# Performance work log

Measured on AMD Instinct MI355X. Metric: run time of the kernel, lower is better.

Reference implementation:

```python
import jax, jax.numpy as jnp
import numpy as np

NUM_NODES = 100000
NUM_REL = 237
D = 200            # entity_out_dim_1 * nheads_GAT_1 = 100*2
C = 50             # conv_out_channels
B = 8192           # batch of (h, r, t) triples


def setup_inputs() -> dict:
    key = jax.random.key(0)
    ks = jax.random.split(key, 8)
    heads = jax.random.randint(ks[0], (B, 1), 0, NUM_NODES)
    rels = jax.random.randint(ks[1], (B, 1), 0, NUM_REL)
    tails = jax.random.randint(ks[2], (B, 1), 0, NUM_NODES)
    batch_inputs = jnp.concatenate([heads, rels, tails], axis=1).astype(jnp.int64)
    return {
        "batch_inputs": batch_inputs,
        "final_entity_embeddings": jax.random.normal(ks[3], (NUM_NODES, D), jnp.float32),
        "final_relation_embeddings": jax.random.normal(ks[4], (NUM_REL, D), jnp.float32),
        "W_ent2rel": jax.random.normal(ks[5], (NUM_REL, D, D), jnp.float32) * (1.0 / np.sqrt(D)),
        "conv_w": jax.random.normal(ks[6], (C, 3), jnp.float32) * 0.5,
        "conv_b": jnp.zeros((C,), jnp.float32),
        "fc_w": jax.random.normal(ks[7], (1, C * D), jnp.float32) * (1.0 / np.sqrt(C * D)),
        "fc_b": jnp.zeros((1,), jnp.float32),
    }


def reference(batch_inputs, final_entity_embeddings, final_relation_embeddings,
              W_ent2rel, conv_w, conv_b, fc_w, fc_b):
    h_idx, r_idx, t_idx = batch_inputs[:, 0], batch_inputs[:, 1], batch_inputs[:, 2]
    src = final_entity_embeddings[h_idx]        # [B, D]
    rel = final_relation_embeddings[r_idx]      # [B, D]
    tail = final_entity_embeddings[t_idx]       # [B, D]
    W = W_ent2rel[r_idx]                        # [B, D, D] per-edge relation transform
    # bmm([B,1,D], [B,D,D]) -> [B,1,D], nonlinearity_ent2rel = tanh
    src = jnp.tanh(jnp.einsum('bd,bde->be', src, W))
    tail = jnp.tanh(jnp.einsum('bd,bde->be', tail, W))
    # ConvKB: stack triple as length-3 sequence, Conv2d kernel (1,3) over seq
    stacked = jnp.stack([src, rel, tail], axis=1)            # [B, 3, D]
    conv = jnp.einsum('bkd,ck->bcd', stacked, conv_w) + conv_b[None, :, None]
    conv = jax.nn.relu(conv)                                  # dropout p=0.0 (eval)
    flat = conv.reshape(conv.shape[0], -1)                    # [B, C*D] (C-major, matches torch view)
    out = flat @ fc_w.T + fc_b                                # [B, 1]
    return out
```

## Files before the change

kernel.cpp:

```cpp
#include <hip/hip_runtime.h>
#include <hip/hip_bf16.h>
#include <math.h>

#define DDIM 200
#define D4   50
#define CCH  50
#define NREL 237
#define MAXE 8
#define MAXR 16
#define NT   256
#define KT   7
#define NTI  13
#define KTKG 28
#define NCOLP 208
#define OSTRIDE 204
#define PACK_UNITS (NREL * KTKG * NCOLP)

typedef __attribute__((ext_vector_type(8))) short bf16x8;
typedef __attribute__((ext_vector_type(4))) float f32x4;

__device__ __forceinline__ uint f2bf(float x) {
    __hip_bfloat16 h = __float2bfloat16(x);
    return (uint)*reinterpret_cast<ushort*>(&h);
}

__global__ __launch_bounds__(256) void packW_kernel(
    const float* __restrict__ W, ushort* __restrict__ Wpk)
{
    const int u = blockIdx.x * 256 + threadIdx.x;
    if (u >= PACK_UNITS) return;
    const int col  = u % NCOLP;
    const int rk   = u / NCOLP;
    const int ktkg = rk % KTKG;
    const int r    = rk / KTKG;
    const int k0   = ktkg * 8;
    uint4 pk = {0u, 0u, 0u, 0u};
    if (col < DDIM) {
        const float* base = W + (size_t)r * DDIM * DDIM + col;
        uint vv[8];
        #pragma unroll
        for (int j = 0; j < 8; ++j) {
            const int k = k0 + j;
            vv[j] = (k < DDIM) ? f2bf(base[(size_t)k * DDIM]) : 0u;
        }
        pk.x = vv[0] | (vv[1] << 16);
        pk.y = vv[2] | (vv[3] << 16);
        pk.z = vv[4] | (vv[5] << 16);
        pk.w = vv[6] | (vv[7] << 16);
    }
    *(uint4*)&Wpk[(size_t)u * 8] = pk;
}

__global__ __launch_bounds__(1024) void relsort_kernel(
    const int* __restrict__ bi, int B, int nblk,
    int* __restrict__ perm, int* __restrict__ blk_r,
    int* __restrict__ blk_start, int* __restrict__ blk_cnt)
{
    __shared__ int hist[NREL];
    __shared__ int offs[NREL];
    __shared__ int wsum[16], wsum2[16];
    const int tid  = threadIdx.x;
    const int lane = tid & 63;
    const int w    = tid >> 6;

    if (tid < NREL) hist[tid] = 0;
    __syncthreads();
    for (int i = tid; i < B; i += 1024)
        atomicAdd(&hist[bi[i * 3 + 1]], 1);
    __syncthreads();

    const int v  = (tid < NREL) ? hist[tid] : 0;
    const int v2 = (tid < NREL) ? (v + MAXE - 1) / MAXE : 0;
    int s = v, s2 = v2;
    #pragma unroll
    for (int off = 1; off < 64; off <<= 1) {
        const int u  = __shfl_up(s,  off, 64);
        const int u2 = __shfl_up(s2, off, 64);
        if (lane >= off) { s += u; s2 += u2; }
    }
    if (lane == 63) { wsum[w] = s; wsum2[w] = s2; }
    __syncthreads();
    int base = 0, base2 = 0;
    for (int i = 0; i < w; ++i) { base += wsum[i]; base2 += wsum2[i]; }
    const int my_off  = base  + s  - v;
    const int my_boff = base2 + s2 - v2;
    if (tid < NREL) offs[tid] = my_off;
    __syncthreads();

    for (int i = tid; i < nblk; i += 1024) blk_cnt[i] = 0;
    if (tid < NREL && v > 0) {
        const int nb = (v + MAXE - 1) / MAXE;
        const int cb = v / nb, ext = v - cb * nb;
        int pos = my_off;
        for (int j = 0; j < nb; ++j) {
            const int c = cb + (j < ext ? 1 : 0);
            blk_r[my_boff + j]     = tid;
            blk_start[my_boff + j] = pos;
            blk_cnt[my_boff + j]   = c;
            pos += c;
        }
    }
    __syncthreads();
    for (int i = tid; i < B; i += 1024) {
        const int pos = atomicAdd(&offs[bi[i * 3 + 1]], 1);
        perm[pos] = i;
    }
}

template <bool PACKED>
__global__ __launch_bounds__(NT) void spkbgat_mfma_kernel(
    const int*   __restrict__ bi,
    const float* __restrict__ ent,
    const float* __restrict__ rel_emb,
    const float* __restrict__ W,
    const ushort* __restrict__ Wpk,
    const float* __restrict__ conv_w,
    const float* __restrict__ conv_b,
    const float* __restrict__ fc_w,
    const float* __restrict__ fc_b,
    const int*   __restrict__ perm,
    const int*   __restrict__ blk_r,
    const int*   __restrict__ blk_start,
    const int*   __restrict__ blk_cnt,
    int nblk,
    float*       __restrict__ out)
{
    __shared__ __align__(16) ushort Ash[KTKG * MAXR * 8];
    __shared__ __align__(16) float  Osh[MAXR][OSTRIDE];
    __shared__ __align__(16) float4 rl4[D4];
    __shared__ __align__(16) float  cwb[CCH][4];
    __shared__ int eid_lds[MAXR];
    __shared__ int bix_lds[MAXE];

    const int tid  = threadIdx.x;
    const int w    = tid >> 6;
    const int lane = tid & 63;
    const int l16  = lane & 15;
    const int kg   = lane >> 4;

    const int bid = blockIdx.x;
    const int q = nblk >> 3, rmd = nblk & 7;
    const int xcd = bid & 7, idx = bid >> 3;
    const int gidx = (xcd < rmd ? xcd * (q + 1) : rmd * (q + 1) + (xcd - rmd) * q) + idx;

    const int cnt = blk_cnt[gidx];
    if (cnt == 0) return;

    const int r     = blk_r[gidx];
    const int start = blk_start[gidx];
    const int rows  = 2 * cnt;

    if (tid < CCH) {
        cwb[tid][0] = conv_w[tid * 3 + 0];
        cwb[tid][1] = conv_w[tid * 3 + 1];
        cwb[tid][2] = conv_w[tid * 3 + 2];
        cwb[tid][3] = conv_b[tid];
    }
    if (tid < D4) rl4[tid] = ((const float4*)rel_emb)[r * D4 + tid];
    if (tid < MAXE) {
        const int b = (tid < cnt) ? perm[start + tid] : -1;
        bix_lds[tid] = b;
        const int bb = (b >= 0) ? b : 0;
        eid_lds[2 * tid]     = bi[3 * bb + 0];
        eid_lds[2 * tid + 1] = bi[3 * bb + 2];
    }
    __syncthreads();

    for (int u = tid; u < KTKG * MAXR; u += NT) {
        const int row  = u & (MAXR - 1);
        const int ktkg = u >> 4;
        uint4 pk = {0u, 0u, 0u, 0u};
        if (ktkg < 25 && row < rows) {
            const float* xp = ent + (size_t)eid_lds[row] * DDIM + ktkg * 8;
            const float4 x0 = *(const float4*)xp;
            const float4 x1 = *(const float4*)(xp + 4);
            pk.x = f2bf(x0.x) | (f2bf(x0.y) << 16);
            pk.y = f2bf(x0.z) | (f2bf(x0.w) << 16);
            pk.z = f2bf(x1.x) | (f2bf(x1.y) << 16);
            pk.w = f2bf(x1.z) | (f2bf(x1.w) << 16);
        }
        *(uint4*)&Ash[u * 8] = pk;
    }
    __syncthreads();

    const int nslots = (w == 0) ? 4 : 3;
    const float*  __restrict__ Wr = W + (size_t)r * DDIM * DDIM;
    const ushort* __restrict__ Wp = Wpk + (size_t)r * KTKG * NCOLP * 8;
    f32x4 acc[4];
    #pragma unroll
    for (int s = 0; s < 4; ++s) acc[s] = (f32x4){0.f, 0.f, 0.f, 0.f};

    for (int kt = 0; kt < KT; ++kt) {
        const int ktkg = kt * 4 + kg;
        const bf16x8 a0 = *(const bf16x8*)&Ash[(ktkg * MAXR + l16) * 8];
        #pragma unroll
        for (int s = 0; s < 4; ++s) {
            if (s < nslots) {
                const int col = (w + 4 * s) * 16 + l16;
                bf16x8 bf;
                if (PACKED) {
                    bf = *(const bf16x8*)&Wp[((size_t)ktkg * NCOLP + col) * 8];
                } else {
                    const int k0 = ktkg * 8;
                    #pragma unroll
                    for (int j = 0; j < 8; ++j) {
                        const int k = k0 + j;
                        const float v = (k < DDIM && col < DDIM) ? Wr[k * DDIM + col] : 0.f;
                        bf[j] = (short)f2bf(v);
                    }
                }
                acc[s] = __builtin_amdgcn_mfma_f32_16x16x32_bf16(a0, bf, acc[s], 0, 0, 0);
            }
        }
    }

    #pragma unroll
    for (int s = 0; s < 4; ++s) {
        if (s < nslots) {
            const int gcol = (w + 4 * s) * 16 + l16;
            if (gcol < DDIM) {
                #pragma unroll
                for (int v = 0; v < 4; ++v) {
                    const int grow = kg * 4 + v;
                    if (grow < rows)
                        Osh[grow][gcol] = tanhf(acc[s][v]);
                }
            }
        }
    }
    __syncthreads();

    float sums[2] = {0.f, 0.f};
    if (lane < D4) {
        const float4 rv = rl4[lane];
        float4 se[2], te[2];
        #pragma unroll
        for (int s2 = 0; s2 < 2; ++s2) {
            const int e = w + 4 * s2;
            if (e < cnt) {
                se[s2] = *(const float4*)&Osh[2 * e][4 * lane];
                te[s2] = *(const float4*)&Osh[2 * e + 1][4 * lane];
            } else {
                se[s2] = (float4){0.f, 0.f, 0.f, 0.f};
                te[s2] = (float4){0.f, 0.f, 0.f, 0.f};
            }
        }
        for (int c = 0; c < CCH; ++c) {
            const float4 cw  = *(const float4*)&cwb[c][0];
            const float4 fc4 = ((const float4*)fc_w)[c * D4 + lane];
            #pragma unroll
            for (int s2 = 0; s2 < 2; ++s2) {
                if (w + 4 * s2 < cnt) {
                    const float v0 = fmaf(cw.x, se[s2].x, fmaf(cw.y, rv.x, fmaf(cw.z, te[s2].x, cw.w)));
                    const float v1 = fmaf(cw.x, se[s2].y, fmaf(cw.y, rv.y, fmaf(cw.z, te[s2].y, cw.w)));
                    const float v2 = fmaf(cw.x, se[s2].z, fmaf(cw.y, rv.z, fmaf(cw.z, te[s2].z, cw.w)));
                    const float v3 = fmaf(cw.x, se[s2].w, fmaf(cw.y, rv.w, fmaf(cw.z, te[s2].w, cw.w)));
                    sums[s2] = fmaf(fmaxf(v0, 0.f), fc4.x, sums[s2]);
                    sums[s2] = fmaf(fmaxf(v1, 0.f), fc4.y, sums[s2]);
                    sums[s2] = fmaf(fmaxf(v2, 0.f), fc4.z, sums[s2]);
                    sums[s2] = fmaf(fmaxf(v3, 0.f), fc4.w, sums[s2]);
                }
            }
        }
    }
    #pragma unroll
    for (int s2 = 0; s2 < 2; ++s2) {
        float v = sums[s2];
        #pragma unroll
        for (int off = 32; off; off >>= 1)
            v += __shfl_down(v, off, 64);
        if (lane == 0) {
            const int e = w + 4 * s2;
            if (e < cnt) out[bix_lds[e]] = v + fc_b[0];
        }
    }
}

extern "C" void kernel_launch(void* const* d_in, const int* in_sizes, int n_in,
                              void* d_out, int out_size, void* d_ws, size_t ws_size,
                              hipStream_t stream) {
    const int*   bi      = (const int*)  d_in[0];
    const float* ent     = (const float*)d_in[1];
    const float* rel_emb = (const float*)d_in[2];
    const float* W       = (const float*)d_in[3];
    const float* conv_w  = (const float*)d_in[4];
    const float* conv_b  = (const float*)d_in[5];
    const float* fc_w    = (const float*)d_in[6];
    const float* fc_b    = (const float*)d_in[7];
    float*       out     = (float*)d_out;

    const int B    = in_sizes[0] / 3;
    const int nblk = NREL + (B + MAXE - 1) / MAXE;

    int* perm      = (int*)d_ws;
    int* blk_r     = perm + B;
    int* blk_start = blk_r + nblk;
    int* blk_cnt   = blk_start + nblk;

    const size_t meta_bytes = (size_t)(B + 3 * nblk) * sizeof(int);
    const size_t pk_off     = (meta_bytes + 255) & ~(size_t)255;
    const size_t need       = pk_off + (size_t)PACK_UNITS * 16;
    const bool   use_packed = (ws_size >= need);
    ushort* Wpk = (ushort*)((char*)d_ws + pk_off);

    if (use_packed) {
        packW_kernel<<<(PACK_UNITS + 255) / 256, 256, 0, stream>>>(W, Wpk);
    }
    relsort_kernel<<<1, 1024, 0, stream>>>(bi, B, nblk, perm, blk_r, blk_start, blk_cnt);
    if (use_packed) {
        spkbgat_mfma_kernel<true><<<nblk, NT, 0, stream>>>(
            bi, ent, rel_emb, W, Wpk, conv_w, conv_b, fc_w, fc_b,
            perm, blk_r, blk_start, blk_cnt, nblk, out);
    } else {
        spkbgat_mfma_kernel<false><<<nblk, NT, 0, stream>>>(
            bi, ent, rel_emb, W, Wpk, conv_w, conv_b, fc_w, fc_b,
            perm, blk_r, blk_start, blk_cnt, nblk, out);
    }
}
```

Baseline: 58.35 us.

## Fuse pack and sort prep kernels, halve edges per block, use fast tanh

Merges the W bf16 packing kernel and the relation-sort kernel into one launch: block 0 sorts and the remaining blocks pack. Halves edges per main-kernel block from 8 to 4, which doubles the grid so each wave handles one edge in the conv/fc epilogue. The A tile is still padded to 16 rows for the MFMA. Replaces tanhf with an exp-based fast tanh. The cost is more blocks re-reading each relation's packed W, and slightly lower tanh accuracy.

```diff
diff --git a/kernel.cpp b/kernel.cpp
--- a/kernel.cpp
+++ b/kernel.cpp
@@ -6,11 +6,11 @@
 #define D4   50
 #define CCH  50
 #define NREL 237
-#define MAXE 8
-#define MAXR 16
+#define MAXE 4
+#define MAXR 8
+#define AROWS 16
 #define NT   256
 #define KT   7
-#define NTI  13
 #define KTKG 28
 #define NCOLP 208
 #define OSTRIDE 204
@@ -24,42 +24,50 @@
     return (uint)*reinterpret_cast<ushort*>(&h);
 }
 
-__global__ __launch_bounds__(256) void packW_kernel(
-    const float* __restrict__ W, ushort* __restrict__ Wpk)
-{
-    const int u = blockIdx.x * 256 + threadIdx.x;
-    if (u >= PACK_UNITS) return;
-    const int col  = u % NCOLP;
-    const int rk   = u / NCOLP;
-    const int ktkg = rk % KTKG;
-    const int r    = rk / KTKG;
-    const int k0   = ktkg * 8;
-    uint4 pk = {0u, 0u, 0u, 0u};
-    if (col < DDIM) {
-        const float* base = W + (size_t)r * DDIM * DDIM + col;
-        uint vv[8];
-        #pragma unroll
-        for (int j = 0; j < 8; ++j) {
-            const int k = k0 + j;
-            vv[j] = (k < DDIM) ? f2bf(base[(size_t)k * DDIM]) : 0u;
-        }
-        pk.x = vv[0] | (vv[1] << 16);
-        pk.y = vv[2] | (vv[3] << 16);
-        pk.z = vv[4] | (vv[5] << 16);
-        pk.w = vv[6] | (vv[7] << 16);
-    }
-    *(uint4*)&Wpk[(size_t)u * 8] = pk;
-}
-
-__global__ __launch_bounds__(1024) void relsort_kernel(
+__device__ __forceinline__ float fast_tanh(float x) {
+    const float xc = fminf(fmaxf(x, -20.f), 20.f);
+    const float e  = __expf(2.f * xc);
+    return 1.f - __fdividef(2.f, e + 1.f);
+}
+
+__global__ __launch_bounds__(1024) void prep_kernel(
+    const float* __restrict__ W, ushort* __restrict__ Wpk, int do_pack,
     const int* __restrict__ bi, int B, int nblk,
     int* __restrict__ perm, int* __restrict__ blk_r,
     int* __restrict__ blk_start, int* __restrict__ blk_cnt)
 {
+    const int tid = threadIdx.x;
+
+    if (blockIdx.x != 0) {
+        if (!do_pack) return;
+        const int u = (blockIdx.x - 1) * 1024 + tid;
+        if (u >= PACK_UNITS) return;
+        const int col  = u % NCOLP;
+        const int rk   = u / NCOLP;
+        const int ktkg = rk % KTKG;
+        const int r    = rk / KTKG;
+        const int k0   = ktkg * 8;
+        uint4 pk = {0u, 0u, 0u, 0u};
+        if (col < DDIM) {
+            const float* base = W + (size_t)r * DDIM * DDIM + col;
+            uint vv[8];
+            #pragma unroll
+            for (int j = 0; j < 8; ++j) {
+                const int k = k0 + j;
+                vv[j] = (k < DDIM) ? f2bf(base[(size_t)k * DDIM]) : 0u;
+            }
+            pk.x = vv[0] | (vv[1] << 16);
+            pk.y = vv[2] | (vv[3] << 16);
+            pk.z = vv[4] | (vv[5] << 16);
+            pk.w = vv[6] | (vv[7] << 16);
+        }
+        *(uint4*)&Wpk[(size_t)u * 8] = pk;
+        return;
+    }
+
     __shared__ int hist[NREL];
     __shared__ int offs[NREL];
     __shared__ int wsum[16], wsum2[16];
-    const int tid  = threadIdx.x;
     const int lane = tid & 63;
     const int w    = tid >> 6;
 
@@ -125,7 +133,7 @@
     int nblk,
     float*       __restrict__ out)
 {
-    __shared__ __align__(16) ushort Ash[KTKG * MAXR * 8];
+    __shared__ __align__(16) ushort Ash[KTKG * AROWS * 8];
     __shared__ __align__(16) float  Osh[MAXR][OSTRIDE];
     __shared__ __align__(16) float4 rl4[D4];
     __shared__ __align__(16) float  cwb[CCH][4];
@@ -166,8 +174,8 @@
     }
     __syncthreads();
 
-    for (int u = tid; u < KTKG * MAXR; u += NT) {
-        const int row  = u & (MAXR - 1);
+    for (int u = tid; u < KTKG * AROWS; u += NT) {
+        const int row  = u & (AROWS - 1);
         const int ktkg = u >> 4;
         uint4 pk = {0u, 0u, 0u, 0u};
         if (ktkg < 25 && row < rows) {
@@ -192,7 +200,7 @@
 
     for (int kt = 0; kt < KT; ++kt) {
         const int ktkg = kt * 4 + kg;
-        const bf16x8 a0 = *(const bf16x8*)&Ash[(ktkg * MAXR + l16) * 8];
+        const bf16x8 a0 = *(const bf16x8*)&Ash[(ktkg * AROWS + l16) * 8];
         #pragma unroll
         for (int s = 0; s < 4; ++s) {
             if (s < nslots) {
@@ -205,8 +213,8 @@
                     #pragma unroll
                     for (int j = 0; j < 8; ++j) {
                         const int k = k0 + j;
-                        const float v = (k < DDIM && col < DDIM) ? Wr[k * DDIM + col] : 0.f;
-                        bf[j] = (short)f2bf(v);
+                        const float vv = (k < DDIM && col < DDIM) ? Wr[k * DDIM + col] : 0.f;
+                        bf[j] = (short)f2bf(vv);
                     }
                 }
                 acc[s] = __builtin_amdgcn_mfma_f32_16x16x32_bf16(a0, bf, acc[s], 0, 0, 0);
@@ -223,57 +231,37 @@
                 for (int v = 0; v < 4; ++v) {
                     const int grow = kg * 4 + v;
                     if (grow < rows)
-                        Osh[grow][gcol] = tanhf(acc[s][v]);
+                        Osh[grow][gcol] = fast_tanh(acc[s][v]);
                 }
             }
         }
     }
     __syncthreads();
 
-    float sums[2] = {0.f, 0.f};
-    if (lane < D4) {
+    float4 sumv = {0.f, 0.f, 0.f, 0.f};
+    const bool live = (w < cnt);
+    if (lane < D4 && live) {
         const float4 rv = rl4[lane];
-        float4 se[2], te[2];
-        #pragma unroll
-        for (int s2 = 0; s2 < 2; ++s2) {
-            const int e = w + 4 * s2;
-            if (e < cnt) {
-                se[s2] = *(const float4*)&Osh[2 * e][4 * lane];
-                te[s2] = *(const float4*)&Osh[2 * e + 1][4 * lane];
-            } else {
-                se[s2] = (float4){0.f, 0.f, 0.f, 0.f};
-                te[s2] = (float4){0.f, 0.f, 0.f, 0.f};
-            }
-        }
+        const float4 se = *(const float4*)&Osh[2 * w][4 * lane];
+        const float4 te = *(const float4*)&Osh[2 * w + 1][4 * lane];
         for (int c = 0; c < CCH; ++c) {
             const float4 cw  = *(const float4*)&cwb[c][0];
             const float4 fc4 = ((const float4*)fc_w)[c * D4 + lane];
-            #pragma unroll
-            for (int s2 = 0; s2 < 2; ++s2) {
-                if (w + 4 * s2 < cnt) {
-                    const float v0 = fmaf(cw.x, se[s2].x, fmaf(cw.y, rv.x, fmaf(cw.z, te[s2].x, cw.w)));
-                    const float v1 = fmaf(cw.x, se[s2].y, fmaf(cw.y, rv.y, fmaf(cw.z, te[s2].y, cw.w)));
-                    const float v2 = fmaf(cw.x, se[s2].z, fmaf(cw.y, rv.z, fmaf(cw.z, te[s2].z, cw.w)));
-                    const float v3 = fmaf(cw.x, se[s2].w, fmaf(cw.y, rv.w, fmaf(cw.z, te[s2].w, cw.w)));
-                    sums[s2] = fmaf(fmaxf(v0, 0.f), fc4.x, sums[s2]);
-                    sums[s2] = fmaf(fmaxf(v1, 0.f), fc4.y, sums[s2]);
-                    sums[s2] = fmaf(fmaxf(v2, 0.f), fc4.z, sums[s2]);
-                    sums[s2] = fmaf(fmaxf(v3, 0.f), fc4.w, sums[s2]);
-                }
-            }
-        }
-    }
+            const float v0 = fmaf(cw.x, se.x, fmaf(cw.y, rv.x, fmaf(cw.z, te.x, cw.w)));
+            const float v1 = fmaf(cw.x, se.y, fmaf(cw.y, rv.y, fmaf(cw.z, te.y, cw.w)));
+            const float v2 = fmaf(cw.x, se.z, fmaf(cw.y, rv.z, fmaf(cw.z, te.z, cw.w)));
+            const float v3 = fmaf(cw.x, se.w, fmaf(cw.y, rv.w, fmaf(cw.z, te.w, cw.w)));
+            sumv.x = fmaf(fmaxf(v0, 0.f), fc4.x, sumv.x);
+            sumv.y = fmaf(fmaxf(v1, 0.f), fc4.y, sumv.y);
+            sumv.z = fmaf(fmaxf(v2, 0.f), fc4.z, sumv.z);
+            sumv.w = fmaf(fmaxf(v3, 0.f), fc4.w, sumv.w);
+        }
+    }
+    float sum = (sumv.x + sumv.y) + (sumv.z + sumv.w);
     #pragma unroll
-    for (int s2 = 0; s2 < 2; ++s2) {
-        float v = sums[s2];
-        #pragma unroll
-        for (int off = 32; off; off >>= 1)
-            v += __shfl_down(v, off, 64);
-        if (lane == 0) {
-            const int e = w + 4 * s2;
-            if (e < cnt) out[bix_lds[e]] = v + fc_b[0];
-        }
-    }
+    for (int off = 32; off; off >>= 1)
+        sum += __shfl_down(sum, off, 64);
+    if (lane == 0 && live) out[bix_lds[w]] = sum + fc_b[0];
 }
 
 extern "C" void kernel_launch(void* const* d_in, const int* in_sizes, int n_in,
@@ -303,10 +291,10 @@
     const bool   use_packed = (ws_size >= need);
     ushort* Wpk = (ushort*)((char*)d_ws + pk_off);
 
-    if (use_packed) {
-        packW_kernel<<<(PACK_UNITS + 255) / 256, 256, 0, stream>>>(W, Wpk);
-    }
-    relsort_kernel<<<1, 1024, 0, stream>>>(bi, B, nblk, perm, blk_r, blk_start, blk_cnt);
+    const int prep_blocks = 1 + (PACK_UNITS + 1023) / 1024;
+    prep_kernel<<<prep_blocks, 1024, 0, stream>>>(
+        W, Wpk, use_packed ? 1 : 0, bi, B, nblk, perm, blk_r, blk_start, blk_cnt);
+
     if (use_packed) {
         spkbgat_mfma_kernel<true><<<nblk, NT, 0, stream>>>(
             bi, ent, rel_emb, W, Wpk, conv_w, conv_b, fc_w, fc_b,
```

New measurement: 57.41 us. No clear change (-1.6%).
